# Optimization experiments

Hardware: AMD Instinct MI355X
Metric: run time of the kernel (lower is better)

## Reference

```python
import jax, jax.numpy as jnp
import numpy as np

N, E, D, H, K = 8192, 8, 1024, 4096, 2


def setup_inputs() -> dict:
    key = jax.random.key(0)
    ks = jax.random.split(key, 12)
    s = 0.02  # init scale for weights
    return {
        "x": jax.random.normal(ks[0], (N, D), jnp.float32),
        "noise": jax.random.normal(ks[1], (N, E), jnp.float32),
        "Wg_w": jax.random.normal(ks[2], (D, E), jnp.float32) * s,
        "Wg_b": jnp.zeros((E,), jnp.float32),
        "Wn_w": jax.random.normal(ks[3], (D, E), jnp.float32) * s,
        "Wn_b": jnp.zeros((E,), jnp.float32),
        "w1": jax.random.normal(ks[4], (E, D, H), jnp.float32) * s,
        "b1": jnp.zeros((E, H), jnp.float32),
        "w2": jax.random.normal(ks[5], (E, H, D), jnp.float32) * s,
        "b2": jnp.zeros((E, D), jnp.float32),
        "k": K,
    }


def reference(x, noise, Wg_w, Wg_b, Wn_w, Wn_b, w1, b1, w2, b2, k):
    # --- noisy top-k gating: H(x) = Wg(x) + noise * softplus(Wn(x)) ---
    g_logits = x @ Wg_w + Wg_b                       # [N, E]
    n_scale = jax.nn.softplus(x @ Wn_w + Wn_b)       # [N, E]
    h = g_logits + noise * n_scale                   # [N, E]
    topk_vals, topk_inds = jax.lax.top_k(h, k)       # [N, k]
    gates = jax.nn.softmax(topk_vals, axis=-1)       # [N, k]

    # Scatter top-k gates into a dense [N, E] map (zeros for unselected experts),
    # so the weighted combine is exactly sum_j gates[n,j] * expert_{inds[n,j]}(x_n).
    n_tok, n_exp = h.shape
    dense_gates = jnp.zeros((n_tok, n_exp), h.dtype).at[
        jnp.arange(n_tok)[:, None], topk_inds
    ].set(gates)                                     # [N, E]

    # --- per-expert 2-layer MLP: fc2(relu(fc1(x))) ---
    hid = jax.nn.relu(jnp.einsum('nd,edh->neh', x, w1) + b1)  # [N, E, H]
    y = jnp.einsum('neh,ehd->ned', hid, w2) + b2              # [N, E, D]
    out = jnp.einsum('ned,ne->nd', y, dense_gates)            # [N, D]
    return out
```

## Files before the change

### kernel.cpp

```cpp
#include <hip/hip_runtime.h>
#include <hip/hip_bf16.h>

#define NTOK 8192
#define NEXP 8
#define DMODEL 1024
#define DHID 4096

typedef __bf16 bf16x8 __attribute__((ext_vector_type(8)));
typedef float f32x4 __attribute__((ext_vector_type(4)));

__device__ __forceinline__ unsigned short f2bf(float f) {
  return __builtin_bit_cast(unsigned short, __float2bfloat16(f));
}

__device__ __forceinline__ void gload_lds16(const void* g, void* l) {
  __builtin_amdgcn_global_load_lds(
      (const __attribute__((address_space(1))) unsigned int*)g,
      (__attribute__((address_space(3))) unsigned int*)l, 16, 0, 0);
}

__device__ __forceinline__ int imin(int a, int b) { return a < b ? a : b; }

constexpr size_t OFF_XB   = 0;
constexpr size_t OFF_W1T  = OFF_XB + (size_t)NTOK * DMODEL * 2;
constexpr size_t OFF_W2T  = OFF_W1T + (size_t)NEXP * DHID * DMODEL * 2;
constexpr size_t OFF_HID  = OFF_W2T + (size_t)NEXP * DMODEL * DHID * 2;
constexpr size_t OFF_IDX  = OFF_HID + (size_t)NTOK * 2 * DHID * 2;
constexpr size_t OFF_GATE = OFF_IDX + (size_t)NTOK * 2 * 4;
constexpr size_t OFF_LIST = OFF_GATE + (size_t)NTOK * 2 * 4;
constexpr size_t OFF_CNT  = OFF_LIST + (size_t)NTOK * 2 * 4;
constexpr size_t OFF_OFFS = OFF_CNT + 128;
constexpr size_t OFF_CUR  = OFF_OFFS + 128;

__global__ void transpose_bf16_kernel(const float* __restrict__ in,
                                      unsigned short* __restrict__ out,
                                      int R, int C) {
  __shared__ float sh[64][65];
  const size_t ebase = (size_t)blockIdx.z * R * C;
  const float* ine = in + ebase;
  unsigned short* oute = out + ebase;
  int c0 = blockIdx.x * 64, r0 = blockIdx.y * 64;
  int tx = threadIdx.x & 15, ty = threadIdx.x >> 4;
#pragma unroll
  for (int p = 0; p < 4; ++p) {
    int row = ty + p * 16;
    float4 v = *(const float4*)&ine[(size_t)(r0 + row) * C + c0 + tx * 4];
    sh[row][tx * 4 + 0] = v.x;
    sh[row][tx * 4 + 1] = v.y;
    sh[row][tx * 4 + 2] = v.z;
    sh[row][tx * 4 + 3] = v.w;
  }
  __syncthreads();
#pragma unroll
  for (int p = 0; p < 4; ++p) {
    int crow = ty + p * 16;
    ushort4 o;
    o.x = f2bf(sh[tx * 4 + 0][crow]);
    o.y = f2bf(sh[tx * 4 + 1][crow]);
    o.z = f2bf(sh[tx * 4 + 2][crow]);
    o.w = f2bf(sh[tx * 4 + 3][crow]);
    *(ushort4*)&oute[(size_t)(c0 + crow) * R + r0 + tx * 4] = o;
  }
}

__global__ void gating_kernel(const float* __restrict__ x,
                              const float* __restrict__ noise,
                              const float* __restrict__ Wg_w,
                              const float* __restrict__ Wg_b,
                              const float* __restrict__ Wn_w,
                              const float* __restrict__ Wn_b,
                              unsigned short* __restrict__ xb,
                              int* __restrict__ topk_idx,
                              float* __restrict__ topk_gate,
                              int* __restrict__ counts) {
  int wave = threadIdx.x >> 6;
  int lane = threadIdx.x & 63;
  int n = blockIdx.x * 4 + wave;
  if (n >= NTOK) return;

  float ag[8] = {0.f, 0.f, 0.f, 0.f, 0.f, 0.f, 0.f, 0.f};
  float an[8] = {0.f, 0.f, 0.f, 0.f, 0.f, 0.f, 0.f, 0.f};
  const float* xr = x + (size_t)n * DMODEL;
  unsigned short* xbr = xb + (size_t)n * DMODEL;
#pragma unroll 4
  for (int i = 0; i < DMODEL / 64; ++i) {
    int d = lane + i * 64;
    float xv = xr[d];
    xbr[d] = f2bf(xv);
    const float4* wg = (const float4*)(Wg_w + (size_t)d * 8);
    const float4* wn = (const float4*)(Wn_w + (size_t)d * 8);
    float4 g0 = wg[0], g1 = wg[1];
    float4 n0 = wn[0], n1 = wn[1];
    ag[0] += xv * g0.x; ag[1] += xv * g0.y; ag[2] += xv * g0.z; ag[3] += xv * g0.w;
    ag[4] += xv * g1.x; ag[5] += xv * g1.y; ag[6] += xv * g1.z; ag[7] += xv * g1.w;
    an[0] += xv * n0.x; an[1] += xv * n0.y; an[2] += xv * n0.z; an[3] += xv * n0.w;
    an[4] += xv * n1.x; an[5] += xv * n1.y; an[6] += xv * n1.z; an[7] += xv * n1.w;
  }
#pragma unroll
  for (int off = 32; off > 0; off >>= 1) {
#pragma unroll
    for (int j = 0; j < 8; ++j) {
      ag[j] += __shfl_down(ag[j], off, 64);
      an[j] += __shfl_down(an[j], off, 64);
    }
  }
  if (lane == 0) {
    float h[8];
#pragma unroll
    for (int e = 0; e < 8; ++e) {
      float gl = ag[e] + Wg_b[e];
      float z = an[e] + Wn_b[e];
      float sp = fmaxf(z, 0.f) + log1pf(expf(-fabsf(z)));
      h[e] = gl + noise[(size_t)n * 8 + e] * sp;
    }
    int i0 = 0; float v0 = h[0];
#pragma unroll
    for (int e = 1; e < 8; ++e)
      if (h[e] > v0) { v0 = h[e]; i0 = e; }
    int i1 = -1; float v1 = -1e30f;
#pragma unroll
    for (int e = 0; e < 8; ++e)
      if (e != i0 && h[e] > v1) { v1 = h[e]; i1 = e; }
    float e1 = expf(v1 - v0);
    float inv = 1.f / (1.f + e1);
    topk_idx[n * 2] = i0;
    topk_idx[n * 2 + 1] = i1;
    topk_gate[n * 2] = inv;
    topk_gate[n * 2 + 1] = e1 * inv;
    atomicAdd(&counts[i0], 1);
    atomicAdd(&counts[i1], 1);
  }
}

__global__ void scan_kernel(const int* __restrict__ counts,
                            int* __restrict__ offsets, int* __restrict__ cursor) {
  if (threadIdx.x == 0) {
    int acc = 0;
    for (int e = 0; e < NEXP; ++e) {
      offsets[e] = acc;
      cursor[e] = acc;
      acc += counts[e];
    }
    offsets[NEXP] = acc;
  }
}

__global__ void scatter_kernel(const int* __restrict__ topk_idx,
                               int* __restrict__ cursor, int* __restrict__ list) {
  int n = blockIdx.x * 256 + threadIdx.x;
  if (n >= NTOK) return;
#pragma unroll
  for (int j = 0; j < 2; ++j) {
    int e = topk_idx[n * 2 + j];
    int pos = atomicAdd(&cursor[e], 1);
    list[pos] = n * 2 + j;
  }
}

#define VMW(N) asm volatile("s_waitcnt vmcnt(" #N ")" ::: "memory")

template <int MODE>
__global__ __launch_bounds__(256, 4) void expert_gemm(
    const unsigned short* __restrict__ Asrc, const unsigned short* __restrict__ Bt,
    const float* __restrict__ bias, const int* __restrict__ offsets,
    const int* __restrict__ list, const float* __restrict__ gates,
    unsigned short* __restrict__ hid, float* __restrict__ out) {
  constexpr int Krow = MODE ? DHID : DMODEL;
  constexpr int Nout = MODE ? DMODEL : DHID;
  constexpr int NT = Krow / 32;

  const int gx = gridDim.x, gy = gridDim.y;
  const int lin = blockIdx.x + gx * (blockIdx.y + gy * blockIdx.z);
  const int e = lin & 7;
  int r = lin >> 3;

  int by, bx;
  if (MODE == 0) {
    int st = r >> 6;
    int inner = r & 63;
    int sm = st >> 2, sn = st & 3;
    if (sm & 1) sn = 3 - sn;
    by = sm * 8 + (inner >> 3);
    bx = sn * 8 + (inner & 7);
  } else {
    by = r & 63;
    bx = r >> 6;
  }

  const int off = offsets[e];
  const int ne = offsets[e + 1] - off;
  const int m0 = by * 128;
  if (m0 >= ne) return;
  const int n0 = bx * 128;

  __shared__ alignas(16) unsigned short Al[2][128 * 32];
  __shared__ alignas(16) unsigned short Bl[2][128 * 32];

  const int tid = threadIdx.x;
  const int lane = tid & 63;
  const int w = tid >> 6;
  const int wm = (w >> 1) * 64;
  const int wn = (w & 1) * 64;
  const int lr = lane & 15;
  const int kg = lane >> 4;
  const int chrd = (kg ^ ((lr >> 1) & 3)) * 8;

  const unsigned short* srcA[2];
  const unsigned short* srcB[2];
#pragma unroll
  for (int i = 0; i < 2; ++i) {
    int q = tid + i * 256;
    int rr = q >> 2, c = q & 3;
    int cs = c ^ ((rr >> 1) & 3);
    int p = off + imin(m0 + rr, ne - 1);
    if (MODE == 0) {
      int token = list[p] >> 1;
      srcA[i] = Asrc + (size_t)token * DMODEL + cs * 8;
    } else {
      srcA[i] = Asrc + (size_t)p * DHID + cs * 8;
    }
    srcB[i] = Bt + (size_t)e * Nout * Krow + (size_t)(n0 + rr) * Krow + cs * 8;
  }

  f32x4 acc[4][4] = {};

  auto stage = [&](int slot, int kt) {
#pragma unroll
    for (int i = 0; i < 2; ++i) {
      int q = tid + i * 256;
      gload_lds16(srcA[i] + kt * 32, &Al[slot][q * 8]);
      gload_lds16(srcB[i] + kt * 32, &Bl[slot][q * 8]);
    }
  };

  auto compute = [&](int slot) {
    bf16x8 af[4], bfr[4];
#pragma unroll
    for (int mf = 0; mf < 4; ++mf)
      af[mf] = *(const bf16x8*)&Al[slot][(wm + mf * 16 + lr) * 32 + chrd];
#pragma unroll
    for (int nf = 0; nf < 4; ++nf)
      bfr[nf] = *(const bf16x8*)&Bl[slot][(wn + nf * 16 + lr) * 32 + chrd];
    asm volatile("s_waitcnt lgkmcnt(0)" ::: "memory");
    __builtin_amdgcn_sched_barrier(0);
#pragma unroll
    for (int mf = 0; mf < 4; ++mf)
#pragma unroll
      for (int nf = 0; nf < 4; ++nf)
        acc[mf][nf] = __builtin_amdgcn_mfma_f32_16x16x32_bf16(af[mf], bfr[nf],
                                                              acc[mf][nf], 0, 0, 0);
  };

  stage(0, 0);
  stage(1, 1);

  int cur = 0;
  for (int t = 0; t < NT; ++t) {
    if (t < NT - 1) { VMW(4); }
    else { VMW(0); }
    __builtin_amdgcn_s_barrier();
    __builtin_amdgcn_sched_barrier(0);
    compute(cur);
    asm volatile("s_waitcnt lgkmcnt(0)" ::: "memory");
    __builtin_amdgcn_sched_barrier(0);
    __builtin_amdgcn_s_barrier();
    if (t + 2 < NT) stage(cur, t + 2);
    cur ^= 1;
  }

  if (MODE == 0) {
#pragma unroll
    for (int mf = 0; mf < 4; ++mf) {
#pragma unroll
      for (int j = 0; j < 4; ++j) {
        int rloc = wm + mf * 16 + kg * 4 + j;
        int row = m0 + rloc;
        if (row < ne) {
          size_t p = (size_t)(off + row);
#pragma unroll
          for (int nf = 0; nf < 4; ++nf) {
            int col = n0 + wn + nf * 16 + lr;
            float v = acc[mf][nf][j] + bias[(size_t)e * Nout + col];
            hid[p * DHID + col] = f2bf(fmaxf(v, 0.f));
          }
        }
      }
    }
  } else {
#pragma unroll
    for (int mf = 0; mf < 4; ++mf) {
#pragma unroll
      for (int j = 0; j < 4; ++j) {
        int rloc = wm + mf * 16 + kg * 4 + j;
        int row = m0 + rloc;
        if (row < ne) {
          int lv = list[off + row];
          int token = lv >> 1;
          float g = gates[lv];
#pragma unroll
          for (int nf = 0; nf < 4; ++nf) {
            int col = n0 + wn + nf * 16 + lr;
            float v = (acc[mf][nf][j] + bias[(size_t)e * Nout + col]) * g;
            atomicAdd(&out[(size_t)token * DMODEL + col], v);
          }
        }
      }
    }
  }
}

extern "C" void kernel_launch(void* const* d_in, const int* in_sizes, int n_in,
                              void* d_out, int out_size, void* d_ws, size_t ws_size,
                              hipStream_t stream) {
  const float* x = (const float*)d_in[0];
  const float* noise = (const float*)d_in[1];
  const float* Wg_w = (const float*)d_in[2];
  const float* Wg_b = (const float*)d_in[3];
  const float* Wn_w = (const float*)d_in[4];
  const float* Wn_b = (const float*)d_in[5];
  const float* w1 = (const float*)d_in[6];
  const float* b1 = (const float*)d_in[7];
  const float* w2 = (const float*)d_in[8];
  const float* b2 = (const float*)d_in[9];
  float* out = (float*)d_out;

  char* ws = (char*)d_ws;
  unsigned short* xb = (unsigned short*)(ws + OFF_XB);
  unsigned short* w1t = (unsigned short*)(ws + OFF_W1T);
  unsigned short* w2t = (unsigned short*)(ws + OFF_W2T);
  unsigned short* hid = (unsigned short*)(ws + OFF_HID);
  int* topk_idx = (int*)(ws + OFF_IDX);
  float* topk_gate = (float*)(ws + OFF_GATE);
  int* list = (int*)(ws + OFF_LIST);
  int* counts = (int*)(ws + OFF_CNT);
  int* offsets = (int*)(ws + OFF_OFFS);
  int* cursor = (int*)(ws + OFF_CUR);

  hipMemsetAsync(out, 0, (size_t)NTOK * DMODEL * sizeof(float), stream);
  hipMemsetAsync(counts, 0, NEXP * sizeof(int), stream);

  transpose_bf16_kernel<<<dim3(DHID / 64, DMODEL / 64, NEXP), 256, 0, stream>>>(
      w1, w1t, DMODEL, DHID);
  transpose_bf16_kernel<<<dim3(DMODEL / 64, DHID / 64, NEXP), 256, 0, stream>>>(
      w2, w2t, DHID, DMODEL);

  gating_kernel<<<NTOK / 4, 256, 0, stream>>>(x, noise, Wg_w, Wg_b, Wn_w, Wn_b,
                                              xb, topk_idx, topk_gate, counts);
  scan_kernel<<<1, 64, 0, stream>>>(counts, offsets, cursor);
  scatter_kernel<<<NTOK / 256, 256, 0, stream>>>(topk_idx, cursor, list);

  expert_gemm<0><<<dim3(32, 64, NEXP), 256, 0, stream>>>(
      xb, w1t, b1, offsets, list, topk_gate, hid, nullptr);
  expert_gemm<1><<<dim3(8, 64, NEXP), 256, 0, stream>>>(
      hid, w2t, b2, offsets, list, topk_gate, nullptr, out);
}
```

Baseline: 833.4 us.

## Triple-buffer expert GEMM LDS pipeline and stage gating weights in LDS

The grouped expert GEMM moves from double to triple LDS buffering, prefetching three k-tiles ahead and adjusting the vmcnt waits. The goal is to hide more global-load latency behind MFMA work. The gating kernel now copies the Wg and Wn weight matrices into shared memory once per block instead of reading them from global memory per element. The cost is more LDS per block (triple buffers, plus 64KB in gating), which can lower occupancy.

```diff
diff --git a/kernel.cpp b/kernel.cpp
--- a/kernel.cpp
+++ b/kernel.cpp
@@ -63,16 +63,22 @@
   }
 }
 
-__global__ void gating_kernel(const float* __restrict__ x,
-                              const float* __restrict__ noise,
-                              const float* __restrict__ Wg_w,
-                              const float* __restrict__ Wg_b,
-                              const float* __restrict__ Wn_w,
-                              const float* __restrict__ Wn_b,
-                              unsigned short* __restrict__ xb,
-                              int* __restrict__ topk_idx,
-                              float* __restrict__ topk_gate,
-                              int* __restrict__ counts) {
+__global__ __launch_bounds__(256) void gating_kernel(
+    const float* __restrict__ x, const float* __restrict__ noise,
+    const float* __restrict__ Wg_w, const float* __restrict__ Wg_b,
+    const float* __restrict__ Wn_w, const float* __restrict__ Wn_b,
+    unsigned short* __restrict__ xb, int* __restrict__ topk_idx,
+    float* __restrict__ topk_gate, int* __restrict__ counts) {
+  __shared__ float wgl[DMODEL * 8];
+  __shared__ float wnl[DMODEL * 8];
+#pragma unroll
+  for (int i = 0; i < 8; ++i) {
+    int q = threadIdx.x + i * 256;
+    *(float4*)&wgl[q * 4] = ((const float4*)Wg_w)[q];
+    *(float4*)&wnl[q * 4] = ((const float4*)Wn_w)[q];
+  }
+  __syncthreads();
+
   int wave = threadIdx.x >> 6;
   int lane = threadIdx.x & 63;
   int n = blockIdx.x * 4 + wave;
@@ -87,8 +93,8 @@
     int d = lane + i * 64;
     float xv = xr[d];
     xbr[d] = f2bf(xv);
-    const float4* wg = (const float4*)(Wg_w + (size_t)d * 8);
-    const float4* wn = (const float4*)(Wn_w + (size_t)d * 8);
+    const float4* wg = (const float4*)&wgl[d * 8];
+    const float4* wn = (const float4*)&wnl[d * 8];
     float4 g0 = wg[0], g1 = wg[1];
     float4 n0 = wn[0], n1 = wn[1];
     ag[0] += xv * g0.x; ag[1] += xv * g0.y; ag[2] += xv * g0.z; ag[3] += xv * g0.w;
@@ -193,8 +199,8 @@
   if (m0 >= ne) return;
   const int n0 = bx * 128;
 
-  __shared__ alignas(16) unsigned short Al[2][128 * 32];
-  __shared__ alignas(16) unsigned short Bl[2][128 * 32];
+  __shared__ alignas(16) unsigned short Al[3][128 * 32];
+  __shared__ alignas(16) unsigned short Bl[3][128 * 32];
 
   const int tid = threadIdx.x;
   const int lane = tid & 63;
@@ -253,10 +259,12 @@
 
   stage(0, 0);
   stage(1, 1);
+  stage(2, 2);
 
   int cur = 0;
   for (int t = 0; t < NT; ++t) {
-    if (t < NT - 1) { VMW(4); }
+    if (t < NT - 2) { VMW(8); }
+    else if (t == NT - 2) { VMW(4); }
     else { VMW(0); }
     __builtin_amdgcn_s_barrier();
     __builtin_amdgcn_sched_barrier(0);
@@ -264,8 +272,8 @@
     asm volatile("s_waitcnt lgkmcnt(0)" ::: "memory");
     __builtin_amdgcn_sched_barrier(0);
     __builtin_amdgcn_s_barrier();
-    if (t + 2 < NT) stage(cur, t + 2);
-    cur ^= 1;
+    if (t + 3 < NT) stage(cur, t + 3);
+    cur = (cur == 2) ? 0 : cur + 1;
   }
 
   if (MODE == 0) {
```

Result: no change. 834.2 us (+0.1%).

## Merge transpose and gating kernels; double the GEMM K-tile to 64

Applied to the files above, without the earlier changes.

Merges the two weight-transpose kernels and the gating kernel into a single prep launch, with block-index ranges deciding which job each block does. The expert GEMM K-tile grows from 32 to 64: shared buffers double, the LDS XOR swizzle is widened to 8 chunks, each stage issues 4 loads per operand, and each barrier pair now covers 32 MFMAs instead of 16. The min-blocks launch bound is dropped, and the doubled LDS footprint may lower occupancy.

```diff
diff --git a/kernel.cpp b/kernel.cpp
--- a/kernel.cpp
+++ b/kernel.cpp
@@ -32,50 +32,65 @@
 constexpr size_t OFF_OFFS = OFF_CNT + 128;
 constexpr size_t OFF_CUR  = OFF_OFFS + 128;
 
-__global__ void transpose_bf16_kernel(const float* __restrict__ in,
-                                      unsigned short* __restrict__ out,
-                                      int R, int C) {
+__global__ __launch_bounds__(256) void prep_kernel(
+    const float* __restrict__ w1, const float* __restrict__ w2,
+    unsigned short* __restrict__ w1t, unsigned short* __restrict__ w2t,
+    const float* __restrict__ x, const float* __restrict__ noise,
+    const float* __restrict__ Wg_w, const float* __restrict__ Wg_b,
+    const float* __restrict__ Wn_w, const float* __restrict__ Wn_b,
+    unsigned short* __restrict__ xb, int* __restrict__ topk_idx,
+    float* __restrict__ topk_gate, int* __restrict__ counts) {
   __shared__ float sh[64][65];
-  const size_t ebase = (size_t)blockIdx.z * R * C;
-  const float* ine = in + ebase;
-  unsigned short* oute = out + ebase;
-  int c0 = blockIdx.x * 64, r0 = blockIdx.y * 64;
-  int tx = threadIdx.x & 15, ty = threadIdx.x >> 4;
-#pragma unroll
-  for (int p = 0; p < 4; ++p) {
-    int row = ty + p * 16;
-    float4 v = *(const float4*)&ine[(size_t)(r0 + row) * C + c0 + tx * 4];
-    sh[row][tx * 4 + 0] = v.x;
-    sh[row][tx * 4 + 1] = v.y;
-    sh[row][tx * 4 + 2] = v.z;
-    sh[row][tx * 4 + 3] = v.w;
-  }
-  __syncthreads();
-#pragma unroll
-  for (int p = 0; p < 4; ++p) {
-    int crow = ty + p * 16;
-    ushort4 o;
-    o.x = f2bf(sh[tx * 4 + 0][crow]);
-    o.y = f2bf(sh[tx * 4 + 1][crow]);
-    o.z = f2bf(sh[tx * 4 + 2][crow]);
-    o.w = f2bf(sh[tx * 4 + 3][crow]);
-    *(ushort4*)&oute[(size_t)(c0 + crow) * R + r0 + tx * 4] = o;
-  }
-}
-
-__global__ void gating_kernel(const float* __restrict__ x,
-                              const float* __restrict__ noise,
-                              const float* __restrict__ Wg_w,
-                              const float* __restrict__ Wg_b,
-                              const float* __restrict__ Wn_w,
-                              const float* __restrict__ Wn_b,
-                              unsigned short* __restrict__ xb,
-                              int* __restrict__ topk_idx,
-                              float* __restrict__ topk_gate,
-                              int* __restrict__ counts) {
+  const int bid = blockIdx.x;
+
+  if (bid < 16384) {
+    const float* in;
+    unsigned short* outp;
+    int R, C, r0, c0;
+    if (bid < 8192) {
+      int e = bid >> 10, rem = bid & 1023;
+      R = DMODEL; C = DHID;
+      in = w1 + (size_t)e * R * C;
+      outp = w1t + (size_t)e * R * C;
+      r0 = (rem >> 6) * 64;
+      c0 = (rem & 63) * 64;
+    } else {
+      int t = bid - 8192;
+      int e = t >> 10, rem = t & 1023;
+      R = DHID; C = DMODEL;
+      in = w2 + (size_t)e * R * C;
+      outp = w2t + (size_t)e * R * C;
+      r0 = (rem >> 4) * 64;
+      c0 = (rem & 15) * 64;
+    }
+    int tx = threadIdx.x & 15, ty = threadIdx.x >> 4;
+#pragma unroll
+    for (int p = 0; p < 4; ++p) {
+      int row = ty + p * 16;
+      float4 v = *(const float4*)&in[(size_t)(r0 + row) * C + c0 + tx * 4];
+      sh[row][tx * 4 + 0] = v.x;
+      sh[row][tx * 4 + 1] = v.y;
+      sh[row][tx * 4 + 2] = v.z;
+      sh[row][tx * 4 + 3] = v.w;
+    }
+    __syncthreads();
+#pragma unroll
+    for (int p = 0; p < 4; ++p) {
+      int crow = ty + p * 16;
+      ushort4 o;
+      o.x = f2bf(sh[tx * 4 + 0][crow]);
+      o.y = f2bf(sh[tx * 4 + 1][crow]);
+      o.z = f2bf(sh[tx * 4 + 2][crow]);
+      o.w = f2bf(sh[tx * 4 + 3][crow]);
+      *(ushort4*)&outp[(size_t)(c0 + crow) * R + r0 + tx * 4] = o;
+    }
+    return;
+  }
+
+  int g = bid - 16384;
   int wave = threadIdx.x >> 6;
   int lane = threadIdx.x & 63;
-  int n = blockIdx.x * 4 + wave;
+  int n = g * 4 + wave;
   if (n >= NTOK) return;
 
   float ag[8] = {0.f, 0.f, 0.f, 0.f, 0.f, 0.f, 0.f, 0.f};
@@ -160,14 +175,14 @@
 #define VMW(N) asm volatile("s_waitcnt vmcnt(" #N ")" ::: "memory")
 
 template <int MODE>
-__global__ __launch_bounds__(256, 4) void expert_gemm(
+__global__ __launch_bounds__(256) void expert_gemm(
     const unsigned short* __restrict__ Asrc, const unsigned short* __restrict__ Bt,
     const float* __restrict__ bias, const int* __restrict__ offsets,
     const int* __restrict__ list, const float* __restrict__ gates,
     unsigned short* __restrict__ hid, float* __restrict__ out) {
   constexpr int Krow = MODE ? DHID : DMODEL;
   constexpr int Nout = MODE ? DMODEL : DHID;
-  constexpr int NT = Krow / 32;
+  constexpr int NT = Krow / 64;
 
   const int gx = gridDim.x, gy = gridDim.y;
   const int lin = blockIdx.x + gx * (blockIdx.y + gy * blockIdx.z);
@@ -193,8 +208,8 @@
   if (m0 >= ne) return;
   const int n0 = bx * 128;
 
-  __shared__ alignas(16) unsigned short Al[2][128 * 32];
-  __shared__ alignas(16) unsigned short Bl[2][128 * 32];
+  __shared__ alignas(16) unsigned short Al[2][128 * 64];
+  __shared__ alignas(16) unsigned short Bl[2][128 * 64];
 
   const int tid = threadIdx.x;
   const int lane = tid & 63;
@@ -203,15 +218,16 @@
   const int wn = (w & 1) * 64;
   const int lr = lane & 15;
   const int kg = lane >> 4;
-  const int chrd = (kg ^ ((lr >> 1) & 3)) * 8;
-
-  const unsigned short* srcA[2];
-  const unsigned short* srcB[2];
-#pragma unroll
-  for (int i = 0; i < 2; ++i) {
+  const int ch0 = ((kg ^ (lr & 7)) * 8);
+  const int ch1 = (((4 + kg) ^ (lr & 7)) * 8);
+
+  const unsigned short* srcA[4];
+  const unsigned short* srcB[4];
+#pragma unroll
+  for (int i = 0; i < 4; ++i) {
     int q = tid + i * 256;
-    int rr = q >> 2, c = q & 3;
-    int cs = c ^ ((rr >> 1) & 3);
+    int rr = q >> 3, c = q & 7;
+    int cs = c ^ (rr & 7);
     int p = off + imin(m0 + rr, ne - 1);
     if (MODE == 0) {
       int token = list[p] >> 1;
@@ -226,29 +242,37 @@
 
   auto stage = [&](int slot, int kt) {
 #pragma unroll
-    for (int i = 0; i < 2; ++i) {
+    for (int i = 0; i < 4; ++i) {
       int q = tid + i * 256;
-      gload_lds16(srcA[i] + kt * 32, &Al[slot][q * 8]);
-      gload_lds16(srcB[i] + kt * 32, &Bl[slot][q * 8]);
+      gload_lds16(srcA[i] + kt * 64, &Al[slot][q * 8]);
+      gload_lds16(srcB[i] + kt * 64, &Bl[slot][q * 8]);
     }
   };
 
   auto compute = [&](int slot) {
-    bf16x8 af[4], bfr[4];
-#pragma unroll
-    for (int mf = 0; mf < 4; ++mf)
-      af[mf] = *(const bf16x8*)&Al[slot][(wm + mf * 16 + lr) * 32 + chrd];
-#pragma unroll
-    for (int nf = 0; nf < 4; ++nf)
-      bfr[nf] = *(const bf16x8*)&Bl[slot][(wn + nf * 16 + lr) * 32 + chrd];
+    bf16x8 af[4][2], bfr[4][2];
+#pragma unroll
+    for (int mf = 0; mf < 4; ++mf) {
+      const unsigned short* base = &Al[slot][(wm + mf * 16 + lr) * 64];
+      af[mf][0] = *(const bf16x8*)(base + ch0);
+      af[mf][1] = *(const bf16x8*)(base + ch1);
+    }
+#pragma unroll
+    for (int nf = 0; nf < 4; ++nf) {
+      const unsigned short* base = &Bl[slot][(wn + nf * 16 + lr) * 64];
+      bfr[nf][0] = *(const bf16x8*)(base + ch0);
+      bfr[nf][1] = *(const bf16x8*)(base + ch1);
+    }
     asm volatile("s_waitcnt lgkmcnt(0)" ::: "memory");
     __builtin_amdgcn_sched_barrier(0);
 #pragma unroll
-    for (int mf = 0; mf < 4; ++mf)
-#pragma unroll
-      for (int nf = 0; nf < 4; ++nf)
-        acc[mf][nf] = __builtin_amdgcn_mfma_f32_16x16x32_bf16(af[mf], bfr[nf],
-                                                              acc[mf][nf], 0, 0, 0);
+    for (int kk = 0; kk < 2; ++kk)
+#pragma unroll
+      for (int mf = 0; mf < 4; ++mf)
+#pragma unroll
+        for (int nf = 0; nf < 4; ++nf)
+          acc[mf][nf] = __builtin_amdgcn_mfma_f32_16x16x32_bf16(
+              af[mf][kk], bfr[nf][kk], acc[mf][nf], 0, 0, 0);
   };
 
   stage(0, 0);
@@ -256,7 +280,7 @@
 
   int cur = 0;
   for (int t = 0; t < NT; ++t) {
-    if (t < NT - 1) { VMW(4); }
+    if (t < NT - 1) { VMW(8); }
     else { VMW(0); }
     __builtin_amdgcn_s_barrier();
     __builtin_amdgcn_sched_barrier(0);
@@ -339,13 +363,9 @@
   hipMemsetAsync(out, 0, (size_t)NTOK * DMODEL * sizeof(float), stream);
   hipMemsetAsync(counts, 0, NEXP * sizeof(int), stream);
 
-  transpose_bf16_kernel<<<dim3(DHID / 64, DMODEL / 64, NEXP), 256, 0, stream>>>(
-      w1, w1t, DMODEL, DHID);
-  transpose_bf16_kernel<<<dim3(DMODEL / 64, DHID / 64, NEXP), 256, 0, stream>>>(
-      w2, w2t, DHID, DMODEL);
-
-  gating_kernel<<<NTOK / 4, 256, 0, stream>>>(x, noise, Wg_w, Wg_b, Wn_w, Wn_b,
-                                              xb, topk_idx, topk_gate, counts);
+  prep_kernel<<<18432, 256, 0, stream>>>(w1, w2, w1t, w2t, x, noise, Wg_w, Wg_b,
+                                         Wn_w, Wn_b, xb, topk_idx, topk_gate,
+                                         counts);
   scan_kernel<<<1, 64, 0, stream>>>(counts, offsets, cursor);
   scatter_kernel<<<NTOK / 256, 256, 0, stream>>>(topk_idx, cursor, list);
 
```

New measurement: 904.4 us. 1.09x slower.
